# Kernel optimization log

Measured on AMD Instinct MI355X. Metric: run time of the kernel, lower is better.

## Reference

```python
import jax, jax.numpy as jnp
import numpy as np

N_NODES = 500000
N_EDGES = 5000000
IN_CH, OUT_CH = 16, 8


def setup_inputs() -> dict:
    key = jax.random.key(0)
    k1, k2, k3, k4, k5 = jax.random.split(key, 5)
    x = jax.random.normal(k1, (N_NODES, IN_CH), dtype=jnp.float32)
    src = jax.random.randint(k2, (N_EDGES,), 0, N_NODES, dtype=jnp.int64)
    dst = jax.random.randint(k3, (N_EDGES,), 0, N_NODES, dtype=jnp.int64)
    edge_index = jnp.stack([src, dst], axis=0)
    # PyG Linear: weight [out, in], Glorot init; GCNConv bias init zeros
    bound = np.sqrt(6.0 / (IN_CH + OUT_CH))
    W = jax.random.uniform(k4, (OUT_CH, IN_CH), dtype=jnp.float32, minval=-bound, maxval=bound)
    b = jnp.zeros((OUT_CH,), dtype=jnp.float32)
    return {"x": x, "edge_index": edge_index, "W": W, "b": b}


def reference(x, edge_index, W, b):
    """GCNConv(16, 8) with defaults: add_self_loops=True, normalize=True, bias.
    out = D^{-1/2} (A + I) D^{-1/2} X W^T + b, scatter by target index."""
    N = x.shape[0]
    loops = jnp.arange(N, dtype=edge_index.dtype)
    src = jnp.concatenate([edge_index[0], loops])  # [E + N]
    dst = jnp.concatenate([edge_index[1], loops])
    # degree of self-loop-augmented graph, accumulated at target nodes
    deg = jax.ops.segment_sum(jnp.ones(src.shape[0], dtype=x.dtype), dst, num_segments=N)
    dinv = jnp.where(deg > 0, jax.lax.rsqrt(deg), jnp.zeros_like(deg))
    norm = dinv[src] * dinv[dst]  # [E + N]
    h = x @ W.T  # [N, OUT_CH]
    msgs = norm[:, None] * h[src]  # gather + scale, [E + N, OUT_CH]
    out = jax.ops.segment_sum(msgs, dst, num_segments=N) + b
    return out
```

## Files before the change

kernel.cpp:

```cpp
#include <hip/hip_runtime.h>
#include <hip/hip_fp16.h>

#define IN_CH 16
#define OUT_CH 8

#define NT 256
#define EPT 24
#define TILE (NT*EPT)
#define NBUK 512
#define BSHIFT 10
#define BNODES 1024
#define BMASK 1023
#define SRCBITS 19
#define SRCMASK 0x7FFFF
#define CAP 11264
#define RPT 44

typedef float __attribute__((ext_vector_type(4))) fv4;

__global__ void __launch_bounds__(NT) k_bin(const int4* __restrict__ src4,
                                            const int4* __restrict__ dst4, int E,
                                            int* __restrict__ gcur,
                                            unsigned* __restrict__ gbuf) {
    __shared__ int hist[NBUK];
    __shared__ int lofs[NBUK];
    __shared__ int gofs[NBUK];
    __shared__ int wsum[4];
    __shared__ unsigned stage[TILE];
    __shared__ unsigned short posb[TILE];

    int t = threadIdx.x;
    long base = (long)blockIdx.x * TILE;
    int cnt = E - (int)base;
    if (cnt > TILE) cnt = TILE;

    for (int j = t; j < NBUK; j += NT) hist[j] = 0;
    __syncthreads();

    unsigned v[EPT];
    int bk[EPT];
    int rk[EPT];
#pragma unroll
    for (int k = 0; k < EPT / 4; k++) {
        int i4 = t + k * NT;
        if (4 * i4 < cnt) {
            int4 s = src4[base / 4 + i4];
            int4 d = dst4[base / 4 + i4];
            int ss[4] = {s.x, s.y, s.z, s.w};
            int dd[4] = {d.x, d.y, d.z, d.w};
#pragma unroll
            for (int j = 0; j < 4; j++) {
                int q = 4 * k + j;
                bk[q] = dd[j] >> BSHIFT;
                v[q] = ((unsigned)(dd[j] & BMASK) << SRCBITS) | (unsigned)ss[j];
                rk[q] = atomicAdd(&hist[bk[q]], 1);
            }
        } else {
#pragma unroll
            for (int j = 0; j < 4; j++) bk[4 * k + j] = -1;
        }
    }
    __syncthreads();

    int a0 = hist[2 * t], a1 = hist[2 * t + 1];
    int ts = a0 + a1;
    int lane = t & 63, wv = t >> 6;
    int inc = ts;
#pragma unroll
    for (int d = 1; d < 64; d <<= 1) {
        int y = __shfl_up(inc, d);
        if (lane >= d) inc += y;
    }
    if (lane == 63) wsum[wv] = inc;
    __syncthreads();
    int wpre = 0;
#pragma unroll
    for (int w = 0; w < 4; w++) wpre += (w < wv) ? wsum[w] : 0;
    int excl = wpre + inc - ts;

    lofs[2 * t] = excl;
    lofs[2 * t + 1] = excl + a0;
    if (a0 > 0) gofs[2 * t] = atomicAdd(&gcur[2 * t], a0) - excl;
    if (a1 > 0) gofs[2 * t + 1] = atomicAdd(&gcur[2 * t + 1], a1) - (excl + a0);
    __syncthreads();

#pragma unroll
    for (int k = 0; k < EPT; k++) {
        if (bk[k] >= 0) {
            int slot = lofs[bk[k]] + rk[k];
            stage[slot] = v[k];
            posb[slot] = (unsigned short)bk[k];
        }
    }
    __syncthreads();

#pragma unroll
    for (int k = 0; k < EPT; k++) {
        int idx = t + k * NT;
        if (idx < cnt) {
            int b2 = posb[idx];
            gbuf[(size_t)b2 * CAP + idx + gofs[b2]] = stage[idx];
        }
    }
}

__global__ void __launch_bounds__(NT) k_degtrans(const unsigned* __restrict__ gbuf,
                                                 const int* __restrict__ gcur,
                                                 const float* __restrict__ x,
                                                 const float* __restrict__ W,
                                                 uint4* __restrict__ hp16, int N) {
    __shared__ int hist[BNODES];
    __shared__ float Ws[OUT_CH * IN_CH];

    int b = blockIdx.x, t = threadIdx.x;
    int cnt = gcur[b];
    const unsigned* p = gbuf + (size_t)b * CAP;

    if (t < OUT_CH * IN_CH) Ws[t] = W[t];
    for (int j = t; j < BNODES; j += NT) hist[j] = 0;
    __syncthreads();

    int n4 = (cnt + 3) >> 2;
    for (int i4 = t; i4 < n4; i4 += NT) {
        uint4 vv = *(const uint4*)(p + 4 * i4);
        unsigned vs[4] = {vv.x, vv.y, vv.z, vv.w};
#pragma unroll
        for (int j = 0; j < 4; j++)
            if (4 * i4 + j < cnt) atomicAdd(&hist[vs[j] >> SRCBITS], 1);
    }
    __syncthreads();

    int n0 = (b << BSHIFT) + 4 * t;
#pragma unroll
    for (int k = 0; k < 4; k++) {
        int n = n0 + k;
        if (n >= N) break;
        float di = rsqrtf(1.0f + (float)hist[4 * t + k]);
        const float4* xp = (const float4*)(x + (size_t)n * IN_CH);
        float4 a0 = xp[0], a1 = xp[1], a2 = xp[2], a3 = xp[3];
        float xi[IN_CH] = {a0.x, a0.y, a0.z, a0.w, a1.x, a1.y, a1.z, a1.w,
                           a2.x, a2.y, a2.z, a2.w, a3.x, a3.y, a3.z, a3.w};
        float h[OUT_CH];
#pragma unroll
        for (int o = 0; o < OUT_CH; o++) {
            float s = 0.0f;
#pragma unroll
            for (int i = 0; i < IN_CH; i++) s += xi[i] * Ws[o * IN_CH + i];
            h[o] = s * di;
        }
        union { uint4 u; __half2 h2[4]; } pk;
        pk.h2[0] = __float22half2_rn(make_float2(h[0], h[1]));
        pk.h2[1] = __float22half2_rn(make_float2(h[2], h[3]));
        pk.h2[2] = __float22half2_rn(make_float2(h[4], h[5]));
        pk.h2[3] = __float22half2_rn(make_float2(h[6], h[7]));
        hp16[n] = pk.u;
    }
}

__device__ __forceinline__ void acc_add(float* a, uint4 g) {
    union { uint4 u; __half2 h2[4]; } pk;
    pk.u = g;
    float2 f0 = __half22float2(pk.h2[0]);
    float2 f1 = __half22float2(pk.h2[1]);
    float2 f2 = __half22float2(pk.h2[2]);
    float2 f3 = __half22float2(pk.h2[3]);
    a[0] += f0.x; a[1] += f0.y; a[2] += f1.x; a[3] += f1.y;
    a[4] += f2.x; a[5] += f2.y; a[6] += f3.x; a[7] += f3.y;
}

__global__ void __launch_bounds__(NT) k_sortgather(const unsigned* __restrict__ gbuf,
                                                   const int* __restrict__ gcur,
                                                   const uint4* __restrict__ hp16,
                                                   const float* __restrict__ bias,
                                                   float* __restrict__ out, int N) {
    __shared__ unsigned sorted[CAP];
    __shared__ int hist[BNODES];
    __shared__ int wsum[4];

    int b = blockIdx.x, t = threadIdx.x;
    int cnt = gcur[b];
    const unsigned* p = gbuf + (size_t)b * CAP;

    for (int j = t; j < BNODES; j += NT) hist[j] = 0;
    __syncthreads();

    unsigned v[RPT];
    int rk[RPT];
#pragma unroll
    for (int k4 = 0; k4 < RPT / 4; k4++) {
        int idx = 4 * t + k4 * 4 * NT;
        uint4 vv = *(const uint4*)(p + idx);
        unsigned vs[4] = {vv.x, vv.y, vv.z, vv.w};
#pragma unroll
        for (int j = 0; j < 4; j++) {
            int k = 4 * k4 + j;
            if (idx + j < cnt) {
                v[k] = vs[j];
                rk[k] = atomicAdd(&hist[v[k] >> SRCBITS], 1);
            }
        }
    }
    __syncthreads();

    int h0 = hist[4 * t], h1 = hist[4 * t + 1], h2 = hist[4 * t + 2], h3 = hist[4 * t + 3];
    int ts = h0 + h1 + h2 + h3;
    int lane = t & 63, wv = t >> 6;
    int inc = ts;
#pragma unroll
    for (int d = 1; d < 64; d <<= 1) {
        int y = __shfl_up(inc, d);
        if (lane >= d) inc += y;
    }
    if (lane == 63) wsum[wv] = inc;
    __syncthreads();
    int wpre = 0;
#pragma unroll
    for (int w = 0; w < 4; w++) wpre += (w < wv) ? wsum[w] : 0;
    int e0 = wpre + inc - ts;
    int e1 = e0 + h0, e2 = e1 + h1, e3 = e2 + h2;
    hist[4 * t] = e0; hist[4 * t + 1] = e1; hist[4 * t + 2] = e2; hist[4 * t + 3] = e3;
    __syncthreads();

#pragma unroll
    for (int k4 = 0; k4 < RPT / 4; k4++) {
#pragma unroll
        for (int j = 0; j < 4; j++) {
            int k = 4 * k4 + j;
            int idx = 4 * t + k4 * 4 * NT + j;
            if (idx < cnt) {
                int slot = hist[v[k] >> SRCBITS] + rk[k];
                sorted[slot] = v[k] & SRCMASK;
            }
        }
    }
    __syncthreads();

    int n0 = (b << BSHIFT) + 4 * t;
    int eS[4] = {e0, e1, e2, e3};
    int hS[4] = {h0, h1, h2, h3};

    float bb[OUT_CH];
#pragma unroll
    for (int o = 0; o < OUT_CH; o++) bb[o] = bias[o];

#pragma unroll
    for (int k = 0; k < 4; k++) {
        int n = n0 + k;
        if (n >= N) break;

        float a[OUT_CH];
        acc_add((float*)a, hp16[n]);
#pragma unroll
        for (int o = 0; o < OUT_CH; o++) a[o] = a[o];
        {
            union { uint4 u; __half2 h2[4]; } pk;
            pk.u = hp16[n];
            float2 f0 = __half22float2(pk.h2[0]);
            float2 f1 = __half22float2(pk.h2[1]);
            float2 f2 = __half22float2(pk.h2[2]);
            float2 f3 = __half22float2(pk.h2[3]);
            a[0] = f0.x; a[1] = f0.y; a[2] = f1.x; a[3] = f1.y;
            a[4] = f2.x; a[5] = f2.y; a[6] = f3.x; a[7] = f3.y;
        }

        int e = eS[k], end = eS[k] + hS[k];
        for (; e + 3 < end; e += 4) {
            unsigned s0 = sorted[e], s1 = sorted[e + 1];
            unsigned s2 = sorted[e + 2], s3 = sorted[e + 3];
            uint4 g0 = hp16[s0];
            uint4 g1 = hp16[s1];
            uint4 g2 = hp16[s2];
            uint4 g3 = hp16[s3];
            acc_add(a, g0); acc_add(a, g1); acc_add(a, g2); acc_add(a, g3);
        }
        for (; e < end; e++) {
            uint4 g0 = hp16[sorted[e]];
            acc_add(a, g0);
        }

        float di = rsqrtf(1.0f + (float)hS[k]);
        fv4 o0, o1;
#pragma unroll
        for (int j = 0; j < 4; j++) {
            o0[j] = a[j] * di + bb[j];
            o1[j] = a[4 + j] * di + bb[4 + j];
        }
        __builtin_nontemporal_store(o0, (fv4*)(out + (size_t)n * OUT_CH));
        __builtin_nontemporal_store(o1, (fv4*)(out + (size_t)n * OUT_CH) + 1);
    }
}

extern "C" void kernel_launch(void* const* d_in, const int* in_sizes, int n_in,
                              void* d_out, int out_size, void* d_ws, size_t ws_size,
                              hipStream_t stream) {
    const float* x  = (const float*)d_in[0];
    const int*   ei = (const int*)d_in[1];
    const float* W  = (const float*)d_in[2];
    const float* b  = (const float*)d_in[3];
    float* out = (float*)d_out;

    const int N = in_sizes[0] / IN_CH;
    const int E = in_sizes[1] / 2;
    const int* src = ei;
    const int* dst = ei + E;

    const int nbuckets = (N + BNODES - 1) >> BSHIFT;

    int*      gcur = (int*)d_ws;
    uint4*    hp16 = (uint4*)(gcur + NBUK);
    unsigned* gbuf = (unsigned*)(hp16 + N);

    const int tiles = (E + TILE - 1) / TILE;

    (void)hipMemsetAsync(gcur, 0, NBUK * sizeof(int), stream);
    k_bin<<<tiles, NT, 0, stream>>>((const int4*)src, (const int4*)dst, E, gcur, gbuf);
    k_degtrans<<<nbuckets, NT, 0, stream>>>(gbuf, gcur, x, W, hp16, N);
    k_sortgather<<<nbuckets, NT, 0, stream>>>(gbuf, gcur, hp16, b, out, N);
}
```

Before: 215.0 us.

## Fuse degree/transform and sort/gather into one cooperative kernel with grid sync

New measurement: 299.7 us. 1.39x slower.

```diff
diff --git a/kernel.cpp b/kernel.cpp
--- a/kernel.cpp
+++ b/kernel.cpp
@@ -1,5 +1,8 @@
 #include <hip/hip_runtime.h>
 #include <hip/hip_fp16.h>
+#include <hip/hip_cooperative_groups.h>
+
+namespace cg = cooperative_groups;
 
 #define IN_CH 16
 #define OUT_CH 8
@@ -104,6 +107,171 @@
     }
 }
 
+__global__ void __launch_bounds__(NT, 3) k_fused(const unsigned* __restrict__ gbuf,
+                                                 const int* __restrict__ gcur,
+                                                 const float* __restrict__ x,
+                                                 const float* __restrict__ W,
+                                                 uint4* __restrict__ hp16,
+                                                 const float* __restrict__ bias,
+                                                 float* __restrict__ out, int N) {
+    __shared__ unsigned sorted[CAP];
+    __shared__ int hist[BNODES];
+    __shared__ float Ws[OUT_CH * IN_CH];
+    __shared__ int wsum[4];
+
+    int b = blockIdx.x, t = threadIdx.x;
+    int cnt = gcur[b];
+    const unsigned* p = gbuf + (size_t)b * CAP;
+
+    if (t < OUT_CH * IN_CH) Ws[t] = W[t];
+    for (int j = t; j < BNODES; j += NT) hist[j] = 0;
+    __syncthreads();
+
+    unsigned v[RPT];
+    int rk[RPT];
+#pragma unroll
+    for (int k4 = 0; k4 < RPT / 4; k4++) {
+        int idx = 4 * t + k4 * 4 * NT;
+        uint4 vv = *(const uint4*)(p + idx);
+        unsigned vs[4] = {vv.x, vv.y, vv.z, vv.w};
+#pragma unroll
+        for (int j = 0; j < 4; j++) {
+            int k = 4 * k4 + j;
+            if (idx + j < cnt) {
+                v[k] = vs[j];
+                rk[k] = atomicAdd(&hist[v[k] >> SRCBITS], 1);
+            }
+        }
+    }
+    __syncthreads();
+
+    int h0 = hist[4 * t], h1 = hist[4 * t + 1], h2 = hist[4 * t + 2], h3 = hist[4 * t + 3];
+    int ts = h0 + h1 + h2 + h3;
+    int lane = t & 63, wv = t >> 6;
+    int inc = ts;
+#pragma unroll
+    for (int d = 1; d < 64; d <<= 1) {
+        int y = __shfl_up(inc, d);
+        if (lane >= d) inc += y;
+    }
+    if (lane == 63) wsum[wv] = inc;
+    __syncthreads();
+    int wpre = 0;
+#pragma unroll
+    for (int w = 0; w < 4; w++) wpre += (w < wv) ? wsum[w] : 0;
+    int e0 = wpre + inc - ts;
+    int e1 = e0 + h0, e2 = e1 + h1, e3 = e2 + h2;
+    hist[4 * t] = e0; hist[4 * t + 1] = e1; hist[4 * t + 2] = e2; hist[4 * t + 3] = e3;
+
+    int n0 = (b << BSHIFT) + 4 * t;
+    int hh[4] = {h0, h1, h2, h3};
+#pragma unroll
+    for (int k = 0; k < 4; k++) {
+        int n = n0 + k;
+        if (n >= N) break;
+        float di = rsqrtf(1.0f + (float)hh[k]);
+        const float4* xp = (const float4*)(x + (size_t)n * IN_CH);
+        float4 a0 = xp[0], a1 = xp[1], a2 = xp[2], a3 = xp[3];
+        float xi[IN_CH] = {a0.x, a0.y, a0.z, a0.w, a1.x, a1.y, a1.z, a1.w,
+                           a2.x, a2.y, a2.z, a2.w, a3.x, a3.y, a3.z, a3.w};
+        float h[OUT_CH];
+#pragma unroll
+        for (int o = 0; o < OUT_CH; o++) {
+            float s = 0.0f;
+#pragma unroll
+            for (int i = 0; i < IN_CH; i++) s += xi[i] * Ws[o * IN_CH + i];
+            h[o] = s * di;
+        }
+        union { uint4 u; __half2 h2[4]; } pk;
+        pk.h2[0] = __float22half2_rn(make_float2(h[0], h[1]));
+        pk.h2[1] = __float22half2_rn(make_float2(h[2], h[3]));
+        pk.h2[2] = __float22half2_rn(make_float2(h[4], h[5]));
+        pk.h2[3] = __float22half2_rn(make_float2(h[6], h[7]));
+        hp16[n] = pk.u;
+    }
+
+    cg::this_grid().sync();
+
+#pragma unroll
+    for (int k4 = 0; k4 < RPT / 4; k4++) {
+#pragma unroll
+        for (int j = 0; j < 4; j++) {
+            int k = 4 * k4 + j;
+            int idx = 4 * t + k4 * 4 * NT + j;
+            if (idx < cnt) {
+                int slot = hist[v[k] >> SRCBITS] + rk[k];
+                sorted[slot] = v[k] & SRCMASK;
+            }
+        }
+    }
+    __syncthreads();
+
+    int eS[4] = {e0, e1, e2, e3};
+
+    float bb[OUT_CH];
+#pragma unroll
+    for (int o = 0; o < OUT_CH; o++) bb[o] = bias[o];
+
+#pragma unroll
+    for (int k = 0; k < 4; k++) {
+        int n = n0 + k;
+        if (n >= N) break;
+
+        float a[OUT_CH];
+        {
+            union { uint4 u; __half2 h2[4]; } pk;
+            pk.u = hp16[n];
+            float2 f0 = __half22float2(pk.h2[0]);
+            float2 f1 = __half22float2(pk.h2[1]);
+            float2 f2 = __half22float2(pk.h2[2]);
+            float2 f3 = __half22float2(pk.h2[3]);
+            a[0] = f0.x; a[1] = f0.y; a[2] = f1.x; a[3] = f1.y;
+            a[4] = f2.x; a[5] = f2.y; a[6] = f3.x; a[7] = f3.y;
+        }
+
+        int e = eS[k], end = eS[k] + hh[k];
+        for (; e + 3 < end; e += 4) {
+            unsigned s0 = sorted[e], s1 = sorted[e + 1];
+            unsigned s2 = sorted[e + 2], s3 = sorted[e + 3];
+            uint4 g0 = hp16[s0];
+            uint4 g1 = hp16[s1];
+            uint4 g2 = hp16[s2];
+            uint4 g3 = hp16[s3];
+            union { uint4 u; __half2 h2[4]; } pk;
+#pragma unroll
+            for (int jj = 0; jj < 4; jj++) {
+                pk.u = (jj == 0) ? g0 : (jj == 1) ? g1 : (jj == 2) ? g2 : g3;
+                float2 f0 = __half22float2(pk.h2[0]);
+                float2 f1 = __half22float2(pk.h2[1]);
+                float2 f2 = __half22float2(pk.h2[2]);
+                float2 f3 = __half22float2(pk.h2[3]);
+                a[0] += f0.x; a[1] += f0.y; a[2] += f1.x; a[3] += f1.y;
+                a[4] += f2.x; a[5] += f2.y; a[6] += f3.x; a[7] += f3.y;
+            }
+        }
+        for (; e < end; e++) {
+            union { uint4 u; __half2 h2[4]; } pk;
+            pk.u = hp16[sorted[e]];
+            float2 f0 = __half22float2(pk.h2[0]);
+            float2 f1 = __half22float2(pk.h2[1]);
+            float2 f2 = __half22float2(pk.h2[2]);
+            float2 f3 = __half22float2(pk.h2[3]);
+            a[0] += f0.x; a[1] += f0.y; a[2] += f1.x; a[3] += f1.y;
+            a[4] += f2.x; a[5] += f2.y; a[6] += f3.x; a[7] += f3.y;
+        }
+
+        float di = rsqrtf(1.0f + (float)hh[k]);
+        fv4 o0, o1;
+#pragma unroll
+        for (int j = 0; j < 4; j++) {
+            o0[j] = a[j] * di + bb[j];
+            o1[j] = a[4 + j] * di + bb[4 + j];
+        }
+        __builtin_nontemporal_store(o0, (fv4*)(out + (size_t)n * OUT_CH));
+        __builtin_nontemporal_store(o1, (fv4*)(out + (size_t)n * OUT_CH) + 1);
+    }
+}
+
 __global__ void __launch_bounds__(NT) k_degtrans(const unsigned* __restrict__ gbuf,
                                                  const int* __restrict__ gcur,
                                                  const float* __restrict__ x,
@@ -157,17 +325,6 @@
     }
 }
 
-__device__ __forceinline__ void acc_add(float* a, uint4 g) {
-    union { uint4 u; __half2 h2[4]; } pk;
-    pk.u = g;
-    float2 f0 = __half22float2(pk.h2[0]);
-    float2 f1 = __half22float2(pk.h2[1]);
-    float2 f2 = __half22float2(pk.h2[2]);
-    float2 f3 = __half22float2(pk.h2[3]);
-    a[0] += f0.x; a[1] += f0.y; a[2] += f1.x; a[3] += f1.y;
-    a[4] += f2.x; a[5] += f2.y; a[6] += f3.x; a[7] += f3.y;
-}
-
 __global__ void __launch_bounds__(NT) k_sortgather(const unsigned* __restrict__ gbuf,
                                                    const int* __restrict__ gcur,
                                                    const uint4* __restrict__ hp16,
@@ -249,9 +406,6 @@
         if (n >= N) break;
 
         float a[OUT_CH];
-        acc_add((float*)a, hp16[n]);
-#pragma unroll
-        for (int o = 0; o < OUT_CH; o++) a[o] = a[o];
         {
             union { uint4 u; __half2 h2[4]; } pk;
             pk.u = hp16[n];
@@ -271,11 +425,27 @@
             uint4 g1 = hp16[s1];
             uint4 g2 = hp16[s2];
             uint4 g3 = hp16[s3];
-            acc_add(a, g0); acc_add(a, g1); acc_add(a, g2); acc_add(a, g3);
+            union { uint4 u; __half2 h2[4]; } pk;
+#pragma unroll
+            for (int jj = 0; jj < 4; jj++) {
+                pk.u = (jj == 0) ? g0 : (jj == 1) ? g1 : (jj == 2) ? g2 : g3;
+                float2 f0 = __half22float2(pk.h2[0]);
+                float2 f1 = __half22float2(pk.h2[1]);
+                float2 f2 = __half22float2(pk.h2[2]);
+                float2 f3 = __half22float2(pk.h2[3]);
+                a[0] += f0.x; a[1] += f0.y; a[2] += f1.x; a[3] += f1.y;
+                a[4] += f2.x; a[5] += f2.y; a[6] += f3.x; a[7] += f3.y;
+            }
         }
         for (; e < end; e++) {
-            uint4 g0 = hp16[sorted[e]];
-            acc_add(a, g0);
+            union { uint4 u; __half2 h2[4]; } pk;
+            pk.u = hp16[sorted[e]];
+            float2 f0 = __half22float2(pk.h2[0]);
+            float2 f1 = __half22float2(pk.h2[1]);
+            float2 f2 = __half22float2(pk.h2[2]);
+            float2 f3 = __half22float2(pk.h2[3]);
+            a[0] += f0.x; a[1] += f0.y; a[2] += f1.x; a[3] += f1.y;
+            a[4] += f2.x; a[5] += f2.y; a[6] += f3.x; a[7] += f3.y;
         }
 
         float di = rsqrtf(1.0f + (float)hS[k]);
@@ -296,7 +466,7 @@
     const float* x  = (const float*)d_in[0];
     const int*   ei = (const int*)d_in[1];
     const float* W  = (const float*)d_in[2];
-    const float* b  = (const float*)d_in[3];
+    const float* bs = (const float*)d_in[3];
     float* out = (float*)d_out;
 
     const int N = in_sizes[0] / IN_CH;
@@ -306,14 +476,24 @@
 
     const int nbuckets = (N + BNODES - 1) >> BSHIFT;
 
-    int*      gcur = (int*)d_ws;
-    uint4*    hp16 = (uint4*)(gcur + NBUK);
+    char* base = (char*)d_ws;
+    int*      gcur = (int*)base;
+    uint4*    hp16 = (uint4*)(base + 4096);
     unsigned* gbuf = (unsigned*)(hp16 + N);
 
     const int tiles = (E + TILE - 1) / TILE;
 
-    (void)hipMemsetAsync(gcur, 0, NBUK * sizeof(int), stream);
+    (void)hipMemsetAsync(gcur, 0, 4096, stream);
     k_bin<<<tiles, NT, 0, stream>>>((const int4*)src, (const int4*)dst, E, gcur, gbuf);
-    k_degtrans<<<nbuckets, NT, 0, stream>>>(gbuf, gcur, x, W, hp16, N);
-    k_sortgather<<<nbuckets, NT, 0, stream>>>(gbuf, gcur, hp16, b, out, N);
+
+    const unsigned* gbuf_c = gbuf;
+    const int* gcur_c = gcur;
+    void* args[] = {(void*)&gbuf_c, (void*)&gcur_c, (void*)&x, (void*)&W,
+                    (void*)&hp16, (void*)&bs, (void*)&out, (void*)&N};
+    hipError_t ce = hipLaunchCooperativeKernel((void*)k_fused, dim3(nbuckets), dim3(NT),
+                                               args, 0, stream);
+    if (ce != hipSuccess) {
+        k_degtrans<<<nbuckets, NT, 0, stream>>>(gbuf, gcur, x, W, hp16, N);
+        k_sortgather<<<nbuckets, NT, 0, stream>>>(gbuf, gcur, hp16, bs, out, N);
+    }
 }
```
